# Kernel optimization log

Hardware: AMD Instinct MI355X
Metric: run time of the kernel (lower is better)

Reference implementation:

```python
import jax, jax.numpy as jnp
import numpy as np

H = 8       # n_heads
N = 128     # n_vars
HEAD = 64   # per-head dim (== __init__ dim)


def setup_inputs() -> dict:
    key = jax.random.key(0)
    k0, k1, k2, k3, k4 = jax.random.split(key, 5)
    B, L = 4, 8192
    D = H * HEAD
    x = jax.random.normal(k0, (B, L, D), dtype=jnp.float32)
    # nn.Linear default init: U(-1/sqrt(fan_in), 1/sqrt(fan_in)), fan_in = HEAD
    s = 1.0 / np.sqrt(HEAD)
    w1 = jax.random.uniform(k1, (HEAD, HEAD), jnp.float32, -s, s)
    b1 = jax.random.uniform(k2, (HEAD,), jnp.float32, -s, s)
    w2 = jax.random.uniform(k3, (HEAD, HEAD), jnp.float32, -s, s)
    b2 = jax.random.uniform(k4, (HEAD,), jnp.float32, -s, s)
    return {"x": x, "w1": w1, "b1": b1, "w2": w2, "b2": b2}


def reference(x, w1, b1, w2, b2):
    B, L, D = x.shape
    P = L // N  # patches per variable
    # (B,L,D) -> (B,H,L,HEAD) -> (B,H,N,P,HEAD)
    xh = x.reshape(B, L, H, HEAD).transpose(0, 2, 1, 3).reshape(B, H, N, P, HEAD)
    q = xh @ w1.T + b1  # proj_1
    k = xh @ w2.T + b2  # proj_2
    # per (b,h,patch) NxN adjacency over variables
    adj = jax.nn.gelu(jnp.einsum('bhixd,bhjxd->bhxij', q, k), approximate=False)
    adj = jax.nn.softmax(adj, axis=-1)
    # dropout is identity in eval mode; F.normalize(p=1): divide by max(L1, eps)
    adj = adj / jnp.maximum(jnp.sum(jnp.abs(adj), axis=-1, keepdims=True), 1e-12)
    out = jnp.einsum('bhxij,bhjxd->bixhd', adj, xh)  # (B,N,P,H,HEAD)
    return out.reshape(B, L, H * HEAD)
```

## Files before the change

kernel.cpp:

```cpp
#include <hip/hip_runtime.h>
#include <math.h>


namespace {
constexpr int H = 8, NV = 128, HEAD = 64, B = 4, L = 8192;
constexpr int P = L / NV;
constexpr int D = H * HEAD;
constexpr int RS = P * D;

constexpr int XT_S = 136;
constexpr int QK_S = 72;
constexpr int A_S  = 136;

typedef _Float16 half8  __attribute__((ext_vector_type(8)));
typedef _Float16 half4v __attribute__((ext_vector_type(4)));
typedef _Float16 half2v __attribute__((ext_vector_type(2)));
typedef float    floatx4 __attribute__((ext_vector_type(4)));

__device__ __forceinline__ floatx4 mfma16(half8 a, half8 b, floatx4 c) {
    return __builtin_amdgcn_mfma_f32_16x16x32_f16(a, b, c, 0, 0, 0);
}

__device__ __forceinline__ half8 cvt8(float4 a, float4 b) {
    half8 r;
    r[0]=(_Float16)a.x; r[1]=(_Float16)a.y; r[2]=(_Float16)a.z; r[3]=(_Float16)a.w;
    r[4]=(_Float16)b.x; r[5]=(_Float16)b.y; r[6]=(_Float16)b.z; r[7]=(_Float16)b.w;
    return r;
}

__global__ __launch_bounds__(256) void pack_w(const float4* __restrict__ w1,
                                              const float4* __restrict__ w2,
                                              half4v* __restrict__ wh) {
    const int t = blockIdx.x * 256 + threadIdx.x;
    const float4 a = w1[t];
    const float4 b = w2[t];
    half4v ha, hb;
    ha[0]=(_Float16)a.x; ha[1]=(_Float16)a.y; ha[2]=(_Float16)a.z; ha[3]=(_Float16)a.w;
    hb[0]=(_Float16)b.x; hb[1]=(_Float16)b.y; hb[2]=(_Float16)b.z; hb[3]=(_Float16)b.w;
    wh[t] = ha;
    wh[1024 + t] = hb;
}

__global__ __launch_bounds__(256, 3) void space_graph_mfma3(
    const float* __restrict__ x, const _Float16* __restrict__ wh,
    const float* __restrict__ b1, const float* __restrict__ b2,
    float* __restrict__ out)
{
    __shared__ _Float16 lds[64 * XT_S + 2 * NV * QK_S];
    _Float16* Xt = lds;
    _Float16* Qh = lds + 64 * XT_S;
    _Float16* Kh = Qh + NV * QK_S;
    _Float16* A  = Qh;

    const int t    = threadIdx.x;
    const int lane = t & 63;
    const int w    = t >> 6;
    const int col  = lane & 15;
    const int quad = lane >> 4;

    const int blk = blockIdx.x;
    const int p = blk & (P - 1);
    const int h = (blk >> 6) & (H - 1);
    const int b = blk >> 9;
    const size_t base = ((size_t)b * L + (size_t)p) * D + (size_t)h * HEAD;

    {
        const int c  = t & 15;
        const int tt = t >> 4;
        #pragma unroll
        for (int it = 0; it < 4; ++it) {
            const int j0 = 2 * (tt + 16 * it);
            const float4 v0 = *(const float4*)(x + base + (size_t)j0 * RS + c * 4);
            const float4 v1 = *(const float4*)(x + base + (size_t)(j0 + 1) * RS + c * 4);
            const float va[4] = {v0.x, v0.y, v0.z, v0.w};
            const float vb[4] = {v1.x, v1.y, v1.z, v1.w};
            #pragma unroll
            for (int q = 0; q < 4; ++q) {
                half2v pr; pr[0] = (_Float16)va[q]; pr[1] = (_Float16)vb[q];
                *(half2v*)&Xt[(4 * c + q) * XT_S + j0] = pr;
            }
        }
    }

    floatx4 qacc[2][4], kacc[2][4];
    #pragma unroll
    for (int mt = 0; mt < 2; ++mt)
        #pragma unroll
        for (int nt = 0; nt < 4; ++nt) { qacc[mt][nt] = (floatx4)0.0f; kacc[mt][nt] = (floatx4)0.0f; }

    half8 axf[2][2];
    #pragma unroll
    for (int mt = 0; mt < 2; ++mt)
        #pragma unroll
        for (int ks = 0; ks < 2; ++ks) {
            const int row = 32 * w + 16 * mt + col;
            const float* src = x + base + (size_t)row * RS + quad * 8 + 32 * ks;
            axf[mt][ks] = cvt8(*(const float4*)src, *(const float4*)(src + 4));
        }

    const _Float16* w1h = wh;
    const _Float16* w2h = wh + HEAD * HEAD;
    #pragma unroll
    for (int ks = 0; ks < 2; ++ks)
        #pragma unroll
        for (int nt = 0; nt < 4; ++nt) {
            const int n = col + 16 * nt, k0 = quad * 8 + 32 * ks;
            const half8 wb1 = *(const half8*)&w1h[n * HEAD + k0];
            const half8 wb2 = *(const half8*)&w2h[n * HEAD + k0];
            #pragma unroll
            for (int mt = 0; mt < 2; ++mt) {
                qacc[mt][nt] = mfma16(axf[mt][ks], wb1, qacc[mt][nt]);
                kacc[mt][nt] = mfma16(axf[mt][ks], wb2, kacc[mt][nt]);
            }
        }

    float bb1[4], bb2[4];
    #pragma unroll
    for (int nt = 0; nt < 4; ++nt) { bb1[nt] = b1[col + 16 * nt]; bb2[nt] = b2[col + 16 * nt]; }
    #pragma unroll
    for (int mt = 0; mt < 2; ++mt)
        #pragma unroll
        for (int r = 0; r < 4; ++r) {
            const int R = 32 * w + 16 * mt + quad * 4 + r;
            _Float16* qrow = &Qh[R * QK_S + col];
            _Float16* krow = &Kh[R * QK_S + col];
            #pragma unroll
            for (int nt = 0; nt < 4; ++nt) {
                qrow[nt * 16] = (_Float16)(qacc[mt][nt][r] + bb1[nt]);
                krow[nt * 16] = (_Float16)(kacc[mt][nt][r] + bb2[nt]);
            }
        }
    __syncthreads();

    floatx4 sacc[2][8];
    #pragma unroll
    for (int mt = 0; mt < 2; ++mt)
        #pragma unroll
        for (int nt = 0; nt < 8; ++nt) sacc[mt][nt] = (floatx4)0.0f;

    #pragma unroll
    for (int ks = 0; ks < 2; ++ks) {
        half8 qaf[2];
        #pragma unroll
        for (int mt = 0; mt < 2; ++mt)
            qaf[mt] = *(const half8*)&Qh[(32 * w + 16 * mt + col) * QK_S + quad * 8 + 32 * ks];
        #pragma unroll
        for (int nt = 0; nt < 8; ++nt) {
            const half8 kbf = *(const half8*)&Kh[(col + 16 * nt) * QK_S + quad * 8 + 32 * ks];
            #pragma unroll
            for (int mt = 0; mt < 2; ++mt)
                sacc[mt][nt] = mfma16(qaf[mt], kbf, sacc[mt][nt]);
        }
    }
    __syncthreads();

    #pragma unroll
    for (int mt = 0; mt < 2; ++mt)
        #pragma unroll
        for (int r = 0; r < 4; ++r) {
            float wv[8]; float rs = 0.f;
            #pragma unroll
            for (int nt = 0; nt < 8; ++nt) {
                const float s  = sacc[mt][nt][r];
                const float u  = s * fmaf(s * s, 0.035677408137f, 0.7978845608f);
                const float em = __expf(-2.0f * u);
                const float g  = s * __builtin_amdgcn_rcpf(1.0f + em);
                const float e  = __expf(g);
                wv[nt] = e; rs += e;
            }
            rs += __shfl_xor(rs, 1); rs += __shfl_xor(rs, 2);
            rs += __shfl_xor(rs, 4); rs += __shfl_xor(rs, 8);
            const float inv = __builtin_amdgcn_rcpf(rs);
            const int R = 32 * w + 16 * mt + quad * 4 + r;
            _Float16* arow = &A[R * A_S + col];
            #pragma unroll
            for (int nt = 0; nt < 8; ++nt)
                arow[nt * 16] = (_Float16)(wv[nt] * inv);
        }

    floatx4 oacc[2][4];
    #pragma unroll
    for (int mt = 0; mt < 2; ++mt)
        #pragma unroll
        for (int nt = 0; nt < 4; ++nt) oacc[mt][nt] = (floatx4)0.0f;

    #pragma unroll
    for (int ks = 0; ks < 4; ++ks) {
        half8 aaf[2];
        #pragma unroll
        for (int mt = 0; mt < 2; ++mt)
            aaf[mt] = *(const half8*)&A[(32 * w + 16 * mt + col) * A_S + quad * 8 + 32 * ks];
        #pragma unroll
        for (int nt = 0; nt < 4; ++nt) {
            const half8 xbf = *(const half8*)&Xt[(col + 16 * nt) * XT_S + quad * 8 + 32 * ks];
            #pragma unroll
            for (int mt = 0; mt < 2; ++mt)
                oacc[mt][nt] = mfma16(aaf[mt], xbf, oacc[mt][nt]);
        }
    }

    #pragma unroll
    for (int mt = 0; mt < 2; ++mt)
        #pragma unroll
        for (int r = 0; r < 4; ++r) {
            const int i = 32 * w + 16 * mt + quad * 4 + r;
            float* orow = out + base + (size_t)i * RS + col;
            #pragma unroll
            for (int nt = 0; nt < 4; ++nt)
                orow[nt * 16] = oacc[mt][nt][r];
        }
}
}

extern "C" void kernel_launch(void* const* d_in, const int* in_sizes, int n_in,
                              void* d_out, int out_size, void* d_ws, size_t ws_size,
                              hipStream_t stream) {
    const float* x  = (const float*)d_in[0];
    const float* w1 = (const float*)d_in[1];
    const float* b1 = (const float*)d_in[2];
    const float* w2 = (const float*)d_in[3];
    const float* b2 = (const float*)d_in[4];
    float* out = (float*)d_out;
    _Float16* wh = (_Float16*)d_ws;

    hipLaunchKernelGGL(pack_w, dim3(4), dim3(256), 0, stream,
                       (const float4*)w1, (const float4*)w2, (half4v*)wh);
    hipLaunchKernelGGL(space_graph_mfma3, dim3(B * H * P), dim3(256), 0, stream,
                       x, wh, b1, b2, out);
}
```

Measured before the change: 149.2 us.

## Fold both projections into one W1^T W2 Gram matrix with bias vectors

```diff
diff --git a/kernel.cpp b/kernel.cpp
--- a/kernel.cpp
+++ b/kernel.cpp
@@ -9,12 +9,11 @@
 constexpr int RS = P * D;
 
 constexpr int XT_S = 136;
-constexpr int QK_S = 72;
-constexpr int A_S  = 136;
+constexpr int TA_S = 72;
 
 typedef _Float16 half8  __attribute__((ext_vector_type(8)));
-typedef _Float16 half4v __attribute__((ext_vector_type(4)));
 typedef _Float16 half2v __attribute__((ext_vector_type(2)));
+typedef __fp16   fp16x2 __attribute__((ext_vector_type(2)));
 typedef float    floatx4 __attribute__((ext_vector_type(4)));
 
 __device__ __forceinline__ floatx4 mfma16(half8 a, half8 b, floatx4 c) {
@@ -22,35 +21,63 @@
 }
 
 __device__ __forceinline__ half8 cvt8(float4 a, float4 b) {
+    fp16x2 p0 = __builtin_amdgcn_cvt_pkrtz(a.x, a.y);
+    fp16x2 p1 = __builtin_amdgcn_cvt_pkrtz(a.z, a.w);
+    fp16x2 p2 = __builtin_amdgcn_cvt_pkrtz(b.x, b.y);
+    fp16x2 p3 = __builtin_amdgcn_cvt_pkrtz(b.z, b.w);
     half8 r;
-    r[0]=(_Float16)a.x; r[1]=(_Float16)a.y; r[2]=(_Float16)a.z; r[3]=(_Float16)a.w;
-    r[4]=(_Float16)b.x; r[5]=(_Float16)b.y; r[6]=(_Float16)b.z; r[7]=(_Float16)b.w;
+    r[0] = (_Float16)p0[0]; r[1] = (_Float16)p0[1];
+    r[2] = (_Float16)p1[0]; r[3] = (_Float16)p1[1];
+    r[4] = (_Float16)p2[0]; r[5] = (_Float16)p2[1];
+    r[6] = (_Float16)p3[0]; r[7] = (_Float16)p3[1];
     return r;
 }
 
-__global__ __launch_bounds__(256) void pack_w(const float4* __restrict__ w1,
-                                              const float4* __restrict__ w2,
-                                              half4v* __restrict__ wh) {
-    const int t = blockIdx.x * 256 + threadIdx.x;
-    const float4 a = w1[t];
-    const float4 b = w2[t];
-    half4v ha, hb;
-    ha[0]=(_Float16)a.x; ha[1]=(_Float16)a.y; ha[2]=(_Float16)a.z; ha[3]=(_Float16)a.w;
-    hb[0]=(_Float16)b.x; hb[1]=(_Float16)b.y; hb[2]=(_Float16)b.z; hb[3]=(_Float16)b.w;
-    wh[t] = ha;
-    wh[1024 + t] = hb;
-}
-
-__global__ __launch_bounds__(256, 3) void space_graph_mfma3(
-    const float* __restrict__ x, const _Float16* __restrict__ wh,
+__global__ __launch_bounds__(256) void pack_g(
+    const float* __restrict__ w1, const float* __restrict__ w2,
     const float* __restrict__ b1, const float* __restrict__ b2,
-    float* __restrict__ out)
+    _Float16* __restrict__ gth, float* __restrict__ g1f,
+    float* __restrict__ g2f, float* __restrict__ cf)
 {
-    __shared__ _Float16 lds[64 * XT_S + 2 * NV * QK_S];
+    const int t = threadIdx.x;
+    if (blockIdx.x == 16) {
+        if (t < 64) {
+            float a = 0.f;
+            #pragma unroll 8
+            for (int n = 0; n < 64; ++n) a = fmaf(w1[n * 64 + t], b2[n], a);
+            g1f[t] = a;
+        } else if (t < 128) {
+            const int d = t - 64;
+            float a = 0.f;
+            #pragma unroll 8
+            for (int n = 0; n < 64; ++n) a = fmaf(w2[n * 64 + d], b1[n], a);
+            g2f[d] = a;
+        } else if (t == 128) {
+            float a = 0.f;
+            for (int n = 0; n < 64; ++n) a = fmaf(b1[n], b2[n], a);
+            cf[0] = a;
+        }
+        return;
+    }
+    const int gid = blockIdx.x * 256 + t;
+    const int d = gid & 63, e = gid >> 6;
+    float a = 0.f;
+    #pragma unroll 8
+    for (int n = 0; n < 64; ++n) a = fmaf(w1[n * 64 + d], w2[n * 64 + e], a);
+    gth[e * 64 + d] = (_Float16)a;
+}
+
+__global__ __launch_bounds__(256, 4) void space_graph_mfma4(
+    const float* __restrict__ x, const _Float16* __restrict__ gth,
+    const float* __restrict__ g1f, const float* __restrict__ g2f,
+    const float* __restrict__ cf, float* __restrict__ out)
+{
+    __shared__ _Float16 lds[64 * XT_S + NV * TA_S];
+    __shared__ float uv[2 * NV];
     _Float16* Xt = lds;
-    _Float16* Qh = lds + 64 * XT_S;
-    _Float16* Kh = Qh + NV * QK_S;
-    _Float16* A  = Qh;
+    _Float16* TA = lds + 64 * XT_S;
+    float* u_lds = uv;
+    float* v_lds = uv + NV;
 
     const int t    = threadIdx.x;
     const int lane = t & 63;
@@ -82,77 +109,99 @@
         }
     }
 
-    floatx4 qacc[2][4], kacc[2][4];
-    #pragma unroll
-    for (int mt = 0; mt < 2; ++mt)
-        #pragma unroll
-        for (int nt = 0; nt < 4; ++nt) { qacc[mt][nt] = (floatx4)0.0f; kacc[mt][nt] = (floatx4)0.0f; }
+    floatx4 tacc[2][4];
+    #pragma unroll
+    for (int mt = 0; mt < 2; ++mt)
+        #pragma unroll
+        for (int nt = 0; nt < 4; ++nt) tacc[mt][nt] = (floatx4)0.0f;
 
     half8 axf[2][2];
-    #pragma unroll
-    for (int mt = 0; mt < 2; ++mt)
-        #pragma unroll
-        for (int ks = 0; ks < 2; ++ks) {
+    float up[2] = {0.f, 0.f}, vp[2] = {0.f, 0.f};
+    #pragma unroll
+    for (int ks = 0; ks < 2; ++ks) {
+        const float4 ga = *(const float4*)(g1f + quad * 8 + 32 * ks);
+        const float4 gb = *(const float4*)(g1f + quad * 8 + 32 * ks + 4);
+        const float4 ha = *(const float4*)(g2f + quad * 8 + 32 * ks);
+        const float4 hb = *(const float4*)(g2f + quad * 8 + 32 * ks + 4);
+        #pragma unroll
+        for (int mt = 0; mt < 2; ++mt) {
             const int row = 32 * w + 16 * mt + col;
             const float* src = x + base + (size_t)row * RS + quad * 8 + 32 * ks;
-            axf[mt][ks] = cvt8(*(const float4*)src, *(const float4*)(src + 4));
-        }
-
-    const _Float16* w1h = wh;
-    const _Float16* w2h = wh + HEAD * HEAD;
+            const float4 v0 = *(const float4*)src;
+            const float4 v1 = *(const float4*)(src + 4);
+            axf[mt][ks] = cvt8(v0, v1);
+            up[mt] += v0.x * ga.x + v0.y * ga.y + v0.z * ga.z + v0.w * ga.w
+                    + v1.x * gb.x + v1.y * gb.y + v1.z * gb.z + v1.w * gb.w;
+            vp[mt] += v0.x * ha.x + v0.y * ha.y + v0.z * ha.z + v0.w * ha.w
+                    + v1.x * hb.x + v1.y * hb.y + v1.z * hb.z + v1.w * hb.w;
+        }
+    }
+
     #pragma unroll
     for (int ks = 0; ks < 2; ++ks)
         #pragma unroll
         for (int nt = 0; nt < 4; ++nt) {
-            const int n = col + 16 * nt, k0 = quad * 8 + 32 * ks;
-            const half8 wb1 = *(const half8*)&w1h[n * HEAD + k0];
-            const half8 wb2 = *(const half8*)&w2h[n * HEAD + k0];
-            #pragma unroll
-            for (int mt = 0; mt < 2; ++mt) {
-                qacc[mt][nt] = mfma16(axf[mt][ks], wb1, qacc[mt][nt]);
-                kacc[mt][nt] = mfma16(axf[mt][ks], wb2, kacc[mt][nt]);
-            }
-        }
-
-    float bb1[4], bb2[4];
-    #pragma unroll
-    for (int nt = 0; nt < 4; ++nt) { bb1[nt] = b1[col + 16 * nt]; bb2[nt] = b2[col + 16 * nt]; }
+            const half8 gb8 = *(const half8*)&gth[(col + 16 * nt) * HEAD + quad * 8 + 32 * ks];
+            #pragma unroll
+            for (int mt = 0; mt < 2; ++mt)
+                tacc[mt][nt] = mfma16(axf[mt][ks], gb8, tacc[mt][nt]);
+        }
+
+    #pragma unroll
+    for (int mt = 0; mt < 2; ++mt) {
+        float uu = up[mt]; uu += __shfl_xor(uu, 16); uu += __shfl_xor(uu, 32);
+        float vv = vp[mt]; vv += __shfl_xor(vv, 16); vv += __shfl_xor(vv, 32);
+        if (quad == 0) u_lds[32 * w + 16 * mt + col] = uu;
+        if (quad == 1) v_lds[32 * w + 16 * mt + col] = vv;
+    }
+
     #pragma unroll
     for (int mt = 0; mt < 2; ++mt)
         #pragma unroll
         for (int r = 0; r < 4; ++r) {
             const int R = 32 * w + 16 * mt + quad * 4 + r;
-            _Float16* qrow = &Qh[R * QK_S + col];
-            _Float16* krow = &Kh[R * QK_S + col];
-            #pragma unroll
-            for (int nt = 0; nt < 4; ++nt) {
-                qrow[nt * 16] = (_Float16)(qacc[mt][nt][r] + bb1[nt]);
-                krow[nt * 16] = (_Float16)(kacc[mt][nt][r] + bb2[nt]);
-            }
+            _Float16* trow = &TA[R * TA_S + col];
+            #pragma unroll
+            for (int nt = 0; nt < 4; ++nt)
+                trow[nt * 16] = (_Float16)(tacc[mt][nt][r]);
         }
     __syncthreads();
 
+    const float cc = cf[0];
+    float ucr[2][4];
+    #pragma unroll
+    for (int mt = 0; mt < 2; ++mt)
+        #pragma unroll
+        for (int r = 0; r < 4; ++r)
+            ucr[mt][r] = u_lds[32 * w + 16 * mt + quad * 4 + r] + cc;
+    float vrow[8];
+    #pragma unroll
+    for (int nt = 0; nt < 8; ++nt) vrow[nt] = v_lds[col + 16 * nt];
+
     floatx4 sacc[2][8];
     #pragma unroll
     for (int mt = 0; mt < 2; ++mt)
         #pragma unroll
-        for (int nt = 0; nt < 8; ++nt) sacc[mt][nt] = (floatx4)0.0f;
+        for (int nt = 0; nt < 8; ++nt)
+            #pragma unroll
+            for (int r = 0; r < 4; ++r)
+                sacc[mt][nt][r] = ucr[mt][r] + vrow[nt];
 
     #pragma unroll
     for (int ks = 0; ks < 2; ++ks) {
-        half8 qaf[2];
+        half8 taf[2];
         #pragma unroll
         for (int mt = 0; mt < 2; ++mt)
-            qaf[mt] = *(const half8*)&Qh[(32 * w + 16 * mt + col) * QK_S + quad * 8 + 32 * ks];
+            taf[mt] = *(const half8*)&TA[(32 * w + 16 * mt + col) * TA_S + quad * 8 + 32 * ks];
         #pragma unroll
         for (int nt = 0; nt < 8; ++nt) {
-            const half8 kbf = *(const half8*)&Kh[(col + 16 * nt) * QK_S + quad * 8 + 32 * ks];
+            const float* bs = x + base + (size_t)(col + 16 * nt) * RS + quad * 8 + 32 * ks;
+            const half8 xb = cvt8(*(const float4*)bs, *(const float4*)(bs + 4));
             #pragma unroll
             for (int mt = 0; mt < 2; ++mt)
-                sacc[mt][nt] = mfma16(qaf[mt], kbf, sacc[mt][nt]);
-        }
-    }
-    __syncthreads();
+                sacc[mt][nt] = mfma16(taf[mt], xb, sacc[mt][nt]);
+        }
+    }
 
     #pragma unroll
     for (int mt = 0; mt < 2; ++mt)
@@ -171,11 +220,19 @@
             rs += __shfl_xor(rs, 1); rs += __shfl_xor(rs, 2);
             rs += __shfl_xor(rs, 4); rs += __shfl_xor(rs, 8);
             const float inv = __builtin_amdgcn_rcpf(rs);
+            #pragma unroll
+            for (int nt = 0; nt < 8; ++nt) sacc[mt][nt][r] = wv[nt] * inv;
+        }
+
+    #pragma unroll
+    for (int mt = 0; mt < 2; ++mt)
+        #pragma unroll
+        for (int r = 0; r < 4; ++r) {
             const int R = 32 * w + 16 * mt + quad * 4 + r;
-            _Float16* arow = &A[R * A_S + col];
-            #pragma unroll
-            for (int nt = 0; nt < 8; ++nt)
-                arow[nt * 16] = (_Float16)(wv[nt] * inv);
+            _Float16* arow = &TA[R * TA_S + col];
+            #pragma unroll
+            for (int nt = 0; nt < 4; ++nt)
+                arow[nt * 16] = (_Float16)(sacc[mt][nt][r]);
         }
 
     floatx4 oacc[2][4];
@@ -185,17 +242,43 @@
         for (int nt = 0; nt < 4; ++nt) oacc[mt][nt] = (floatx4)0.0f;
 
     #pragma unroll
-    for (int ks = 0; ks < 4; ++ks) {
+    for (int kh = 0; kh < 2; ++kh) {
         half8 aaf[2];
         #pragma unroll
         for (int mt = 0; mt < 2; ++mt)
-            aaf[mt] = *(const half8*)&A[(32 * w + 16 * mt + col) * A_S + quad * 8 + 32 * ks];
+            aaf[mt] = *(const half8*)&TA[(32 * w + 16 * mt + col) * TA_S + quad * 8 + 32 * kh];
         #pragma unroll
         for (int nt = 0; nt < 4; ++nt) {
-            const half8 xbf = *(const half8*)&Xt[(col + 16 * nt) * XT_S + quad * 8 + 32 * ks];
+            const half8 xb = *(const half8*)&Xt[(col + 16 * nt) * XT_S + quad * 8 + 32 * kh];
             #pragma unroll
             for (int mt = 0; mt < 2; ++mt)
-                oacc[mt][nt] = mfma16(aaf[mt], xbf, oacc[mt][nt]);
+                oacc[mt][nt] = mfma16(aaf[mt], xb, oacc[mt][nt]);
+        }
+    }
+
+    #pragma unroll
+    for (int mt = 0; mt < 2; ++mt)
+        #pragma unroll
+        for (int r = 0; r < 4; ++r) {
+            const int R = 32 * w + 16 * mt + quad * 4 + r;
+            _Float16* arow = &TA[R * TA_S + col];
+            #pragma unroll
+            for (int nt = 4; nt < 8; ++nt)
+                arow[(nt - 4) * 16] = (_Float16)(sacc[mt][nt][r]);
+        }
+
+    #pragma unroll
+    for (int kh = 0; kh < 2; ++kh) {
+        half8 aaf[2];
+        #pragma unroll
+        for (int mt = 0; mt < 2; ++mt)
+            aaf[mt] = *(const half8*)&TA[(32 * w + 16 * mt + col) * TA_S + quad * 8 + 32 * kh];
+        #pragma unroll
+        for (int nt = 0; nt < 4; ++nt) {
+            const half8 xb = *(const half8*)&Xt[(col + 16 * nt) * XT_S + quad * 8 + 32 * (kh + 2)];
+            #pragma unroll
+            for (int mt = 0; mt < 2; ++mt)
+                oacc[mt][nt] = mfma16(aaf[mt], xb, oacc[mt][nt]);
         }
     }
 
@@ -221,10 +304,14 @@
     const float* w2 = (const float*)d_in[3];
     const float* b2 = (const float*)d_in[4];
     float* out = (float*)d_out;
-    _Float16* wh = (_Float16*)d_ws;
-
-    hipLaunchKernelGGL(pack_w, dim3(4), dim3(256), 0, stream,
-                       (const float4*)w1, (const float4*)w2, (half4v*)wh);
-    hipLaunchKernelGGL(space_graph_mfma3, dim3(B * H * P), dim3(256), 0, stream,
-                       x, wh, b1, b2, out);
-}
+
+    _Float16* gth = (_Float16*)d_ws;
+    float* g1f = (float*)((char*)d_ws + 8192);
+    float* g2f = g1f + 64;
+    float* cf  = g2f + 64;
+
+    hipLaunchKernelGGL(pack_g, dim3(17), dim3(256), 0, stream,
+                       w1, w2, b1, b2, gth, g1f, g2f, cf);
+    hipLaunchKernelGGL(space_graph_mfma4, dim3(B * H * P), dim3(256), 0, stream,
+                       x, gth, g1f, g2f, cf, out);
+}
```

Measured after the change: 170.1 us. 14.0% more time.
